# Optimization experiments

Measured on AMD Instinct MI355X. Metric: run time of the kernel, lower is better.

The kernel has to match this reference:

```python
import jax, jax.numpy as jnp
import numpy as np

B, S, H, R, DEPTH = 64, 32, 1024, 256, 9  # batch, seq, hidden, GRU hidden (h//reduction), tree depth


def _gru(x, h, W_ih, W_hh, b_ih, b_hh):
    # PyTorch nn.GRUCell math
    gi = x @ W_ih.T + b_ih
    gh = h @ W_hh.T + b_hh
    i_r, i_z, i_n = jnp.split(gi, 3, axis=-1)
    h_r, h_z, h_n = jnp.split(gh, 3, axis=-1)
    r = jax.nn.sigmoid(i_r + h_r)
    z = jax.nn.sigmoid(i_z + h_z)
    n = jnp.tanh(i_n + r * h_n)
    return (1.0 - z) * n + z * h


def _forward(x, W_hidden, b_hidden, W_hb, b_hb, W_branch, b_branch, W_ih, W_hh, b_ih, b_hh, tree_depth):
    selu = jax.nn.selu
    # root: discretize(selu(hidden(selu(x)))).mean over sequence; discretize=identity (discretize kw None)
    xc = selu(selu(x) @ W_hidden.T + b_hidden).mean(axis=1)[:, None, :]  # [B,1,H]
    hc = jnp.zeros((x.shape[0], 1, W_hh.shape[1]), x.dtype)              # [B,1,R]
    depth = jnp.zeros((x.shape[0], 1, 1), x.dtype)
    for _ in range(tree_depth):  # level-synchronous expansion of the recursive generate()
        hc = _gru(xc, hc, W_ih, W_hh, b_ih, b_hh)
        xh = jnp.concatenate([xc, hc], axis=-1)                          # [B,N,H+R]
        hb = jax.nn.sigmoid(xh @ W_hb.T + b_hb)                          # [B,N,1]
        depth = depth + hb
        lr = selu(xh @ W_branch.T + b_branch)                            # [B,N,2H]
        l, r = jnp.split(lr, 2, axis=-1)
        l = xc - selu(l @ W_hidden.T + b_hidden)                          # residual left child
        r = xc - selu(r @ W_hidden.T + b_hidden)                          # residual right child
        Bn, N, Hd = xc.shape
        xc = jnp.stack([l, r], axis=2).reshape(Bn, 2 * N, Hd)
        hc = jnp.repeat(hc, 2, axis=1)
        depth = jnp.repeat(depth, 2, axis=1)
    # leaf nodes: final controller step; terminal = x (no V head), depth += has_branches
    hc = _gru(xc, hc, W_ih, W_hh, b_ih, b_hh)
    hb = jax.nn.sigmoid(jnp.concatenate([xc, hc], axis=-1) @ W_hb.T + b_hb)
    depth = depth + hb
    return jnp.concatenate([xc, depth], axis=-1)  # [B, 2**D, H+1]: leaf terminals + leaf depths


def setup_inputs() -> dict:
    key = jax.random.key(0)
    ks = jax.random.split(key, 6)
    def w(k, o, i):
        return (jax.random.normal(k, (o, i), jnp.float32) / np.sqrt(i)).astype(jnp.float32)
    return {
        'x': jax.random.normal(ks[0], (B, S, H), jnp.float32),
        'W_hidden': w(ks[1], H, H), 'b_hidden': jnp.zeros((H,), jnp.float32),
        'W_hb': w(ks[2], 1, H + R), 'b_hb': jnp.zeros((1,), jnp.float32),
        'W_branch': w(ks[3], 2 * H, H + R), 'b_branch': jnp.zeros((2 * H,), jnp.float32),
        'W_ih': w(ks[4], 3 * R, H), 'W_hh': w(ks[5], 3 * R, R),
        'b_ih': jnp.zeros((3 * R,), jnp.float32), 'b_hh': jnp.zeros((3 * R,), jnp.float32),
        'tree_depth': DEPTH,
    }


def reference(x, W_hidden, b_hidden, W_hb, b_hb, W_branch, b_branch, W_ih, W_hh, b_ih, b_hh, tree_depth):
    return _forward(x, W_hidden, b_hidden, W_hb, b_hb, W_branch, b_branch, W_ih, W_hh, b_ih, b_hh, tree_depth)
```

## Files before the change

### kernel.cpp

```cpp
#include <hip/hip_runtime.h>
#include <hip/hip_bf16.h>
#include <cstdint>
#include <cstddef>


#define SELU_L 1.0507009873554805f
#define SELU_A 1.6732632423543772f

__device__ __forceinline__ float selu_f(float x) {
    return x > 0.f ? SELU_L * x : (SELU_L * SELU_A) * (__expf(x) - 1.f);
}
__device__ __forceinline__ float sigmoid_f(float x) {
    return 1.f / (1.f + __expf(-x));
}

typedef __attribute__((ext_vector_type(8))) short s16x8;
typedef __attribute__((ext_vector_type(4))) float f32x4;

__device__ __forceinline__ void gld16(const void* g, void* l) {
    __builtin_amdgcn_global_load_lds(
        (const __attribute__((address_space(1))) uint32_t*)g,
        (__attribute__((address_space(3))) uint32_t*)l, 16, 0, 0);
}

enum { AM_PLAIN = 0, AM_CONCAT = 2 };
enum { EP_NONE = 0, EP_SELU32 = 1, EP_BRANCH = 2, EP_RESID = 3 };

template <int AMODE, int EPI>
__device__ __forceinline__ void gemm_body(
    int bm, int bn, int M, int K,
    const __hip_bfloat16* __restrict__ A, int lda,
    const __hip_bfloat16* __restrict__ A2,
    const __hip_bfloat16* __restrict__ W,
    const float* __restrict__ bias,
    void* __restrict__ Cv, int ldc,
    const __hip_bfloat16* __restrict__ P,
    float* __restrict__ C32, int ldc32,
    short* As, short* Bs)
{
    const int tid  = threadIdx.x;
    const int wave = tid >> 6;
    const int lane = tid & 63;

    const short* gA[4]; const short* gA2p[4]; const short* gB[4];
    short* dA[4]; short* dB[4];
#pragma unroll
    for (int r = 0; r < 4; ++r) {
        const int s   = r * 256 + wave * 64 + lane;
        const int row = s >> 3;
        const int pc  = s & 7;
        const int j   = (pc - (row >> 1)) & 7;
        const int ga  = min(bm + row, M - 1);
        if (AMODE == AM_CONCAT) {
            gA[r]   = (const short*)A  + (size_t)ga * 1024 + j * 8;
            gA2p[r] = (const short*)A2 + (size_t)ga * 256  + j * 8;
        } else {
            gA[r]   = (const short*)A + (size_t)ga * lda + j * 8;
            gA2p[r] = nullptr;
        }
        gB[r] = (const short*)W + (size_t)(bn + row) * K + j * 8;
        dA[r] = &As[(size_t)(r * 256 + wave * 64) * 8];
        dB[r] = &Bs[(size_t)(r * 256 + wave * 64) * 8];
    }

    const int wm = (wave >> 1) * 64, wn = (wave & 1) * 64;
    const int l16 = lane & 15, q4 = lane >> 4;
    int aoff[4], boff[4];
#pragma unroll
    for (int i = 0; i < 4; ++i) {
        int ra = wm + i * 16 + l16;
        aoff[i] = ra * 64 + (((q4 + (ra >> 1)) & 7) << 3);
        int rb = wn + i * 16 + l16;
        boff[i] = rb * 64 + (((q4 + (rb >> 1)) & 7) << 3);
    }

    f32x4 acc[4][4] = {};

    for (int k0 = 0; k0 < K; k0 += 64) {
#pragma unroll
        for (int r = 0; r < 4; ++r) {
            const short* ap;
            if (AMODE == AM_CONCAT)
                ap = (k0 < 1024) ? gA[r] + k0 : gA2p[r] + (k0 - 1024);
            else
                ap = gA[r] + k0;
            gld16(ap, dA[r]);
            gld16(gB[r] + k0, dB[r]);
        }
        __syncthreads();

#pragma unroll
        for (int h = 0; h < 2; ++h) {
            const int hx = h << 5;
            s16x8 af[4], bf[4];
#pragma unroll
            for (int i = 0; i < 4; ++i) af[i] = *(const s16x8*)&As[aoff[i] ^ hx];
#pragma unroll
            for (int i = 0; i < 4; ++i) bf[i] = *(const s16x8*)&Bs[boff[i] ^ hx];
#pragma unroll
            for (int mi = 0; mi < 4; ++mi)
#pragma unroll
                for (int ni = 0; ni < 4; ++ni)
                    acc[mi][ni] = __builtin_amdgcn_mfma_f32_16x16x32_bf16(
                        af[mi], bf[ni], acc[mi][ni], 0, 0, 0);
        }
        __syncthreads();
    }

    const int crow0 = bm + wm + q4 * 4;
    const int ccol0 = bn + wn + l16;
#pragma unroll
    for (int mi = 0; mi < 4; ++mi) {
#pragma unroll
        for (int r = 0; r < 4; ++r) {
            const int row = crow0 + mi * 16 + r;
            if (row >= M) continue;
#pragma unroll
            for (int ni = 0; ni < 4; ++ni) {
                const int col = ccol0 + ni * 16;
                float v = acc[mi][ni][r] + bias[col];
                if (EPI == EP_NONE) {
                    ((float*)Cv)[(size_t)row * ldc + col] = v;
                } else if (EPI == EP_SELU32) {
                    ((float*)Cv)[(size_t)row * ldc + col] = selu_f(v);
                } else if (EPI == EP_BRANCH) {
                    const int c = col >> 10, jj = col & 1023;
                    ((__hip_bfloat16*)Cv)[(size_t)(2 * row + c) * 1024 + jj] =
                        __float2bfloat16(selu_f(v));
                } else {
                    const float pv = __bfloat162float(P[(size_t)(row >> 1) * 1024 + col]);
                    const float o = pv - selu_f(v);
                    ((__hip_bfloat16*)Cv)[(size_t)row * 1024 + col] = __float2bfloat16(o);
                    if (C32) C32[(size_t)row * ldc32 + col] = o;
                }
            }
        }
    }
}

template <int AMODE, int EPI>
__global__ __launch_bounds__(256) void mgemm(
    int M, int N, int K,
    const __hip_bfloat16* __restrict__ A, int lda,
    const __hip_bfloat16* __restrict__ A2,
    const __hip_bfloat16* __restrict__ W,
    const float* __restrict__ bias,
    void* __restrict__ Cv, int ldc,
    const __hip_bfloat16* __restrict__ P,
    float* __restrict__ C32, int ldc32)
{
    __shared__ short As[8192];
    __shared__ short Bs[8192];
    int bxi = blockIdx.x, byi = blockIdx.y;
    {
        const int ncol = gridDim.x, nrow = gridDim.y;
        if ((nrow & 7) == 0) {
            const int lin = byi * ncol + bxi;
            const int xcd = lin & 7;
            const int t = lin >> 3;
            const int rows_per = nrow >> 3;
            bxi = t % ncol;
            byi = xcd * rows_per + t / ncol;
        }
    }
    gemm_body<AMODE, EPI>(byi * 128, bxi * 128, M, K, A, lda, A2, W, bias,
                          Cv, ldc, P, C32, ldc32, As, Bs);
}

struct GPair {
    int M0, K0; const __hip_bfloat16* A0; int lda0;
    const __hip_bfloat16* W0; const float* b0; float* C0; int ldc0;
    int M1, K1; const __hip_bfloat16* A1; int lda1;
    const __hip_bfloat16* W1; const float* b1; float* C1; int ldc1;
};
__global__ __launch_bounds__(256) void mgemm_pair(GPair g)
{
    __shared__ short As[8192];
    __shared__ short Bs[8192];
    int bxi = blockIdx.x, byi = blockIdx.y;
    if (blockIdx.z == 0) {
        const int ncol = gridDim.x, nrow = gridDim.y;
        if ((nrow & 7) == 0) {
            const int lin = byi * ncol + bxi;
            const int xcd = lin & 7;
            const int t = lin >> 3;
            const int rows_per = nrow >> 3;
            bxi = t % ncol;
            byi = xcd * rows_per + t / ncol;
        }
        gemm_body<AM_PLAIN, EP_NONE>(byi * 128, bxi * 128, g.M0, g.K0,
                                     g.A0, g.lda0, nullptr, g.W0, g.b0,
                                     g.C0, g.ldc0, nullptr, nullptr, 0, As, Bs);
    } else {
        if (byi * 128 >= g.M1) return;
        gemm_body<AM_PLAIN, EP_NONE>(byi * 128, bxi * 128, g.M1, g.K1,
                                     g.A1, g.lda1, nullptr, g.W1, g.b1,
                                     g.C1, g.ldc1, nullptr, nullptr, 0, As, Bs);
    }
}

template <int AMODE, int EPI>
__device__ __forceinline__ void gemm256_body(
    int bm, int bn, int M, int K,
    const __hip_bfloat16* __restrict__ A, int lda,
    const __hip_bfloat16* __restrict__ A2,
    const __hip_bfloat16* __restrict__ W,
    const float* __restrict__ bias,
    void* __restrict__ Cv, int ldc,
    const __hip_bfloat16* __restrict__ P,
    float* __restrict__ C32, int ldc32,
    short* As, short* Bs)
{
    const int tid  = threadIdx.x;
    const int wave = tid >> 6;
    const int lane = tid & 63;
    const int wm = (wave >> 2) * 128;
    const int wn = (wave & 3) * 64;
    const int l16 = lane & 15, q4 = lane >> 4;

    const short* gA[2]; const short* gA2p[2]; const short* gB[2];
    int dOf[2];
#pragma unroll
    for (int r = 0; r < 2; ++r) {
        const int s   = r * 512 + tid;
        const int row = s >> 2;
        const int pc  = s & 3;
        const int j   = (pc - (row >> 1)) & 3;
        const int ga  = min(bm + row, M - 1);
        if (AMODE == AM_CONCAT) {
            gA[r]   = (const short*)A  + (size_t)ga * 1024 + j * 8;
            gA2p[r] = (const short*)A2 + (size_t)ga * 256  + j * 8;
        } else {
            gA[r]   = (const short*)A + (size_t)ga * lda + j * 8;
            gA2p[r] = nullptr;
        }
        gB[r]  = (const short*)W + (size_t)(bn + row) * K + j * 8;
        dOf[r] = (r * 512 + wave * 64) * 8;
    }

    int aof[8], bof[4];
#pragma unroll
    for (int m = 0; m < 8; ++m) {
        const int ra = wm + m * 16 + l16;
        aof[m] = ra * 32 + (((q4 + (ra >> 1)) & 3) << 3);
    }
#pragma unroll
    for (int n = 0; n < 4; ++n) {
        const int rb = wn + n * 16 + l16;
        bof[n] = rb * 32 + (((q4 + (rb >> 1)) & 3) << 3);
    }

    f32x4 acc[8][4] = {};
    const int NT = K >> 5;

    auto stage = [&](int t) {
        const int k0 = t << 5;
        const int sb = (t & 3) << 13;
#pragma unroll
        for (int r = 0; r < 2; ++r) {
            const short* ap;
            if (AMODE == AM_CONCAT)
                ap = (k0 < 1024) ? gA[r] + k0 : gA2p[r] + (k0 - 1024);
            else
                ap = gA[r] + k0;
            gld16(ap, &As[sb + dOf[r]]);
        }
#pragma unroll
        for (int r = 0; r < 2; ++r) gld16(gB[r] + k0, &Bs[sb + dOf[r]]);
    };

    stage(0); stage(1); stage(2);

#define STEP256(t_, DOISS_, VMS_) do {                                        \
        asm volatile("s_waitcnt vmcnt(" VMS_ ")" ::: "memory");               \
        __builtin_amdgcn_s_barrier();                                         \
        asm volatile("" ::: "memory");      \
        const int cur_ = ((t_) & 3) << 13;                                    \
        s16x8 af_[8], bf_[4];                                                 \
        _Pragma("unroll")                                                     \
        for (int m = 0; m < 8; ++m) af_[m] = *(const s16x8*)&As[cur_ + aof[m]]; \
        _Pragma("unroll")                                                     \
        for (int n = 0; n < 4; ++n) bf_[n] = *(const s16x8*)&Bs[cur_ + bof[n]]; \
        if (DOISS_) stage((t_) + 3);                                          \
        __builtin_amdgcn_s_setprio(1);                                        \
        _Pragma("unroll")                                                     \
        for (int m = 0; m < 8; ++m)                                           \
            _Pragma("unroll")                                                 \
            for (int n = 0; n < 4; ++n)                                       \
                acc[m][n] = __builtin_amdgcn_mfma_f32_16x16x32_bf16(          \
                    af_[m], bf_[n], acc[m][n], 0, 0, 0);                      \
        __builtin_amdgcn_s_setprio(0);                                        \
    } while (0)

    for (int t = 0; t < NT - 3; ++t) STEP256(t, 1, "8");
    STEP256(NT - 3, 0, "8");
    STEP256(NT - 2, 0, "4");
    STEP256(NT - 1, 0, "0");
#undef STEP256

    const int crow0 = bm + wm + q4 * 4;
    const int ccol0 = bn + wn + l16;
#pragma unroll
    for (int m8 = 0; m8 < 8; ++m8) {
#pragma unroll
        for (int r = 0; r < 4; ++r) {
            const int row = crow0 + m8 * 16 + r;
            if (row >= M) continue;
#pragma unroll
            for (int n4 = 0; n4 < 4; ++n4) {
                const int col = ccol0 + n4 * 16;
                float v = acc[m8][n4][r] + bias[col];
                if (EPI == EP_NONE) {
                    ((float*)Cv)[(size_t)row * ldc + col] = v;
                } else if (EPI == EP_SELU32) {
                    ((float*)Cv)[(size_t)row * ldc + col] = selu_f(v);
                } else if (EPI == EP_BRANCH) {
                    const int c = col >> 10, jj = col & 1023;
                    ((__hip_bfloat16*)Cv)[(size_t)(2 * row + c) * 1024 + jj] =
                        __float2bfloat16(selu_f(v));
                } else {
                    const float pv = __bfloat162float(P[(size_t)(row >> 1) * 1024 + col]);
                    const float o = pv - selu_f(v);
                    ((__hip_bfloat16*)Cv)[(size_t)row * 1024 + col] = __float2bfloat16(o);
                    if (C32) C32[(size_t)row * ldc32 + col] = o;
                }
            }
        }
    }
}

template <int AMODE, int EPI>
__global__ __launch_bounds__(512) void mgemm256(
    int M, int N, int K,
    const __hip_bfloat16* __restrict__ A, int lda,
    const __hip_bfloat16* __restrict__ A2,
    const __hip_bfloat16* __restrict__ W,
    const float* __restrict__ bias,
    void* __restrict__ Cv, int ldc,
    const __hip_bfloat16* __restrict__ P,
    float* __restrict__ C32, int ldc32)
{
    __shared__ short As[32768];
    __shared__ short Bs[32768];
    int bxi = blockIdx.x, byi = blockIdx.y;
    {
        const int ncol = gridDim.x, nrow = gridDim.y;
        if ((nrow & 7) == 0) {
            const int lin = byi * ncol + bxi;
            const int xcd = lin & 7;
            const int t = lin >> 3;
            const int rows_per = nrow >> 3;
            bxi = t % ncol;
            byi = xcd * rows_per + t / ncol;
        }
    }
    gemm256_body<AMODE, EPI>(byi * 256, bxi * 256, M, K, A, lda, A2, W, bias,
                             Cv, ldc, P, C32, ldc32, As, Bs);
}

__global__ void cvt4_k(const float* __restrict__ s0, __hip_bfloat16* __restrict__ d0, int n0,
                       const float* __restrict__ s1, __hip_bfloat16* __restrict__ d1, int n1,
                       const float* __restrict__ s2, __hip_bfloat16* __restrict__ d2, int n2,
                       const float* __restrict__ s3, __hip_bfloat16* __restrict__ d3, int n3)
{
    int i = blockIdx.x * 256 + threadIdx.x;
    if (i < n0) { d0[i] = __float2bfloat16(s0[i]); return; }
    i -= n0;
    if (i < n1) { d1[i] = __float2bfloat16(s1[i]); return; }
    i -= n1;
    if (i < n2) { d2[i] = __float2bfloat16(s2[i]); return; }
    i -= n2;
    if (i < n3) { d3[i] = __float2bfloat16(s3[i]); }
}

__global__ void selu_cvt_k(const float* __restrict__ in, __hip_bfloat16* __restrict__ out, int n)
{
    int i = blockIdx.x * 256 + threadIdx.x;
    if (i < n) out[i] = __float2bfloat16(selu_f(in[i]));
}

__global__ void mean_kernel(const float* __restrict__ T, __hip_bfloat16* __restrict__ xc)
{
    const int idx = blockIdx.x * 256 + threadIdx.x;
    const int b = idx >> 10, h = idx & 1023;
    const float* p = T + (size_t)b * 32 * 1024 + h;
    float s = 0.f;
#pragma unroll
    for (int si = 0; si < 32; ++si) s += p[si * 1024];
    xc[idx] = __float2bfloat16(s * (1.f / 32.f));
}

__global__ __launch_bounds__(256) void gateshb_kernel(
    const float* __restrict__ gi,
    const float* __restrict__ gh,
    const float* __restrict__ b_hh,
    const __hip_bfloat16* __restrict__ hold,
    __hip_bfloat16* __restrict__ hnew,
    const __hip_bfloat16* __restrict__ xc,
    const float* __restrict__ W_hb,
    const float* __restrict__ b_hb,
    const float* __restrict__ depth_old,
    float* __restrict__ depth_out, int dstride,
    int first)
{
    const int m = blockIdx.x;
    const int j = threadIdx.x;
    __shared__ float red[4];

    const float* gim = gi + (size_t)m * 768;
    const float ir = gim[j], iz = gim[256 + j], in_ = gim[512 + j];
    float hr, hz, hn, h0;
    if (first) {
        hr = b_hh[j]; hz = b_hh[256 + j]; hn = b_hh[512 + j]; h0 = 0.f;
    } else {
        const float* ghm = gh + (size_t)(m >> 1) * 768;
        hr = ghm[j]; hz = ghm[256 + j]; hn = ghm[512 + j];
        h0 = __bfloat162float(hold[(size_t)(m >> 1) * 256 + j]);
    }
    const float r = sigmoid_f(ir + hr);
    const float z = sigmoid_f(iz + hz);
    const float n = tanhf(in_ + r * hn);
    const float hv = (1.f - z) * n + z * h0;
    hnew[(size_t)m * 256 + j] = __float2bfloat16(hv);

    const __hip_bfloat16* xr = xc + (size_t)m * 1024;
    float s = hv * W_hb[1024 + j];
#pragma unroll
    for (int kk = 0; kk < 4; ++kk) {
        const int k = j + kk * 256;
        s += __bfloat162float(xr[k]) * W_hb[k];
    }
#pragma unroll
    for (int off = 32; off; off >>= 1) s += __shfl_down(s, off);
    if ((j & 63) == 0) red[j >> 6] = s;
    __syncthreads();
    if (j == 0) {
        const float tot = red[0] + red[1] + red[2] + red[3];
        const float hb = sigmoid_f(tot + b_hb[0]);
        const float d0 = first ? 0.f : depth_old[m >> 1];
        depth_out[(size_t)m * dstride] = d0 + hb;
    }
}

extern "C" void kernel_launch(void* const* d_in, const int* in_sizes, int n_in,
                              void* d_out, int out_size, void* d_ws, size_t ws_size,
                              hipStream_t stream)
{
    const float* x        = (const float*)d_in[0];
    const float* W_hidden = (const float*)d_in[1];
    const float* b_hidden = (const float*)d_in[2];
    const float* W_hb     = (const float*)d_in[3];
    const float* b_hb     = (const float*)d_in[4];
    const float* W_branch = (const float*)d_in[5];
    const float* b_branch = (const float*)d_in[6];
    const float* W_ih     = (const float*)d_in[7];
    const float* W_hh     = (const float*)d_in[8];
    const float* b_ih     = (const float*)d_in[9];
    const float* b_hh     = (const float*)d_in[10];

    char* ws = (char*)d_ws;
    size_t off = 0;
    auto alloc = [&](size_t bytes) {
        void* p = ws + off;
        off += (bytes + 255) & ~(size_t)255;
        return p;
    };
    __hip_bfloat16* Whb  = (__hip_bfloat16*)alloc(1024 * 1024 * 2);
    __hip_bfloat16* Wbb  = (__hip_bfloat16*)alloc(2048 * 1280 * 2);
    __hip_bfloat16* Wib  = (__hip_bfloat16*)alloc(768 * 1024 * 2);
    __hip_bfloat16* Whh  = (__hip_bfloat16*)alloc(768 * 256 * 2);
    __hip_bfloat16* Xs   = (__hip_bfloat16*)alloc((size_t)2048 * 1024 * 2);
    float*          GI   = (float*)alloc((size_t)32768 * 768 * 4);
    __hip_bfloat16* U    = (__hip_bfloat16*)alloc((size_t)32768 * 1024 * 2);
    __hip_bfloat16* XC0  = (__hip_bfloat16*)alloc((size_t)32768 * 1024 * 2);
    __hip_bfloat16* XC1  = (__hip_bfloat16*)alloc((size_t)32768 * 1024 * 2);
    __hip_bfloat16* HC0  = (__hip_bfloat16*)alloc((size_t)32768 * 256 * 2);
    __hip_bfloat16* HC1  = (__hip_bfloat16*)alloc((size_t)32768 * 256 * 2);
    float*          D0   = (float*)alloc(32768 * 4);
    float*          D1   = (float*)alloc(32768 * 4);
    float*          GH   = (float*)U;

    float* out = (float*)d_out;

    {
        const int n0 = 1024 * 1024, n1 = 2048 * 1280, n2 = 768 * 1024, n3 = 768 * 256;
        cvt4_k<<<(n0 + n1 + n2 + n3 + 255) / 256, 256, 0, stream>>>(
            W_hidden, Whb, n0, W_branch, Wbb, n1, W_ih, Wib, n2, W_hh, Whh, n3);
    }
    selu_cvt_k<<<(2048 * 1024 + 255) / 256, 256, 0, stream>>>(x, Xs, 2048 * 1024);

    mgemm<AM_PLAIN, EP_SELU32><<<dim3(1024 / 128, 2048 / 128), 256, 0, stream>>>(
        2048, 1024, 1024, Xs, 1024, nullptr, Whb, b_hidden, GI, 1024, nullptr, nullptr, 0);
    mean_kernel<<<(64 * 1024) / 256, 256, 0, stream>>>(GI, XC0);

    __hip_bfloat16* xc_cur = XC0; __hip_bfloat16* xc_next = XC1;
    __hip_bfloat16* hc_prev = nullptr; __hip_bfloat16* hc_new = HC0;
    float* d_prev = nullptr; float* d_next = D0;

    for (int d = 0; d < 9; ++d) {
        const int M = 64 << d;
        GPair g;
        g.M0 = M;     g.K0 = 1024; g.A0 = xc_cur;  g.lda0 = 1024;
        g.W0 = Wib;   g.b0 = b_ih; g.C0 = GI;      g.ldc0 = 768;
        g.M1 = M / 2; g.K1 = 256;  g.A1 = hc_prev; g.lda1 = 256;
        g.W1 = Whh;   g.b1 = b_hh; g.C1 = GH;      g.ldc1 = 768;
        mgemm_pair<<<dim3(768 / 128, (M + 127) / 128, d > 0 ? 2 : 1), 256, 0, stream>>>(g);

        gateshb_kernel<<<M, 256, 0, stream>>>(
            GI, (const float*)GH, b_hh, hc_prev, hc_new,
            xc_cur, W_hb, b_hb, d_prev, d_next, 1, d == 0 ? 1 : 0);

        if (d >= 7) {
            mgemm256<AM_CONCAT, EP_BRANCH><<<dim3(2048 / 256, M / 256), 512, 0, stream>>>(
                M, 2048, 1280, xc_cur, 1024, hc_new, Wbb, b_branch, U, 1024,
                nullptr, nullptr, 0);
            mgemm256<AM_PLAIN, EP_RESID><<<dim3(1024 / 256, (2 * M) / 256), 512, 0, stream>>>(
                2 * M, 1024, 1024, U, 1024, nullptr, Whb, b_hidden, xc_next, 1024,
                xc_cur, d == 8 ? out : nullptr, 1025);
        } else {
            mgemm<AM_CONCAT, EP_BRANCH><<<dim3(2048 / 128, (M + 127) / 128), 256, 0, stream>>>(
                M, 2048, 1280, xc_cur, 1024, hc_new, Wbb, b_branch, U, 1024,
                nullptr, nullptr, 0);
            mgemm<AM_PLAIN, EP_RESID><<<dim3(1024 / 128, (2 * M) / 128), 256, 0, stream>>>(
                2 * M, 1024, 1024, U, 1024, nullptr, Whb, b_hidden, xc_next, 1024,
                xc_cur, d == 8 ? out : nullptr, 1025);
        }

        __hip_bfloat16* t = xc_cur; xc_cur = xc_next; xc_next = t;
        hc_prev = hc_new; hc_new = (hc_new == HC0) ? HC1 : HC0;
        d_prev = d_next;  d_next = (d_next == D0) ? D1 : D0;
    }

    {
        const int M = 32768;
        mgemm256<AM_PLAIN, EP_NONE><<<dim3(768 / 256, M / 256), 512, 0, stream>>>(
            M, 768, 1024, xc_cur, 1024, nullptr, Wib, b_ih, GI, 768,
            nullptr, nullptr, 0);
        mgemm<AM_PLAIN, EP_NONE><<<dim3(768 / 128, (M / 2) / 128), 256, 0, stream>>>(
            M / 2, 768, 256, hc_prev, 256, nullptr, Whh, b_hh, (void*)GH, 768,
            nullptr, nullptr, 0);
        gateshb_kernel<<<M, 256, 0, stream>>>(
            GI, (const float*)GH, b_hh, hc_prev, hc_new,
            xc_cur, W_hb, b_hb, d_prev, out + 1024, 1025, 0);
    }
}
```

Baseline: 1.469 ms.

## Fuse tree levels 0-4 into one persistent kernel with grid barriers

```diff
diff --git a/kernel.cpp b/kernel.cpp
--- a/kernel.cpp
+++ b/kernel.cpp
@@ -274,7 +274,7 @@
 #define STEP256(t_, DOISS_, VMS_) do {                                        \
         asm volatile("s_waitcnt vmcnt(" VMS_ ")" ::: "memory");               \
         __builtin_amdgcn_s_barrier();                                         \
-        asm volatile("" ::: "memory");      \
+        asm volatile("" ::: "memory");                                        \
         const int cur_ = ((t_) & 3) << 13;                                    \
         s16x8 af_[8], bf_[4];                                                 \
         _Pragma("unroll")                                                     \
@@ -358,55 +358,17 @@
                              Cv, ldc, P, C32, ldc32, As, Bs);
 }
 
-__global__ void cvt4_k(const float* __restrict__ s0, __hip_bfloat16* __restrict__ d0, int n0,
-                       const float* __restrict__ s1, __hip_bfloat16* __restrict__ d1, int n1,
-                       const float* __restrict__ s2, __hip_bfloat16* __restrict__ d2, int n2,
-                       const float* __restrict__ s3, __hip_bfloat16* __restrict__ d3, int n3)
-{
-    int i = blockIdx.x * 256 + threadIdx.x;
-    if (i < n0) { d0[i] = __float2bfloat16(s0[i]); return; }
-    i -= n0;
-    if (i < n1) { d1[i] = __float2bfloat16(s1[i]); return; }
-    i -= n1;
-    if (i < n2) { d2[i] = __float2bfloat16(s2[i]); return; }
-    i -= n2;
-    if (i < n3) { d3[i] = __float2bfloat16(s3[i]); }
-}
-
-__global__ void selu_cvt_k(const float* __restrict__ in, __hip_bfloat16* __restrict__ out, int n)
-{
-    int i = blockIdx.x * 256 + threadIdx.x;
-    if (i < n) out[i] = __float2bfloat16(selu_f(in[i]));
-}
-
-__global__ void mean_kernel(const float* __restrict__ T, __hip_bfloat16* __restrict__ xc)
-{
-    const int idx = blockIdx.x * 256 + threadIdx.x;
-    const int b = idx >> 10, h = idx & 1023;
-    const float* p = T + (size_t)b * 32 * 1024 + h;
-    float s = 0.f;
-#pragma unroll
-    for (int si = 0; si < 32; ++si) s += p[si * 1024];
-    xc[idx] = __float2bfloat16(s * (1.f / 32.f));
-}
-
-__global__ __launch_bounds__(256) void gateshb_kernel(
-    const float* __restrict__ gi,
-    const float* __restrict__ gh,
+__device__ __forceinline__ void gates_row(
+    int m, int first,
+    const float* __restrict__ gi, const float* __restrict__ gh,
     const float* __restrict__ b_hh,
-    const __hip_bfloat16* __restrict__ hold,
-    __hip_bfloat16* __restrict__ hnew,
+    const __hip_bfloat16* __restrict__ hold, __hip_bfloat16* __restrict__ hnew,
     const __hip_bfloat16* __restrict__ xc,
-    const float* __restrict__ W_hb,
-    const float* __restrict__ b_hb,
-    const float* __restrict__ depth_old,
-    float* __restrict__ depth_out, int dstride,
-    int first)
-{
-    const int m = blockIdx.x;
+    const float* __restrict__ W_hb, const float* __restrict__ b_hb,
+    const float* __restrict__ depth_old, float* __restrict__ depth_out,
+    int dstride, float* red)
+{
     const int j = threadIdx.x;
-    __shared__ float red[4];
-
     const float* gim = gi + (size_t)m * 768;
     const float ir = gim[j], iz = gim[256 + j], in_ = gim[512 + j];
     float hr, hz, hn, h0;
@@ -440,6 +402,153 @@
         const float d0 = first ? 0.f : depth_old[m >> 1];
         depth_out[(size_t)m * dstride] = d0 + hb;
     }
+    __syncthreads();
+}
+
+__global__ __launch_bounds__(256) void gateshb_kernel(
+    const float* __restrict__ gi, const float* __restrict__ gh,
+    const float* __restrict__ b_hh,
+    const __hip_bfloat16* __restrict__ hold, __hip_bfloat16* __restrict__ hnew,
+    const __hip_bfloat16* __restrict__ xc,
+    const float* __restrict__ W_hb, const float* __restrict__ b_hb,
+    const float* __restrict__ depth_old, float* __restrict__ depth_out,
+    int dstride, int first)
+{
+    __shared__ float red[4];
+    gates_row(blockIdx.x, first, gi, gh, b_hh, hold, hnew, xc, W_hb, b_hb,
+              depth_old, depth_out, dstride, red);
+}
+
+__device__ __forceinline__ void grid_barrier(unsigned* bar)
+{
+    __syncthreads();
+    if (threadIdx.x == 0) {
+        __threadfence();
+        const unsigned gen = __hip_atomic_load(&bar[1], __ATOMIC_RELAXED,
+                                               __HIP_MEMORY_SCOPE_AGENT);
+        const unsigned n = __hip_atomic_fetch_add(&bar[0], 1u, __ATOMIC_ACQ_REL,
+                                                  __HIP_MEMORY_SCOPE_AGENT);
+        if (n + 1u == gridDim.x) {
+            __hip_atomic_store(&bar[0], 0u, __ATOMIC_RELAXED,
+                               __HIP_MEMORY_SCOPE_AGENT);
+            __hip_atomic_fetch_add(&bar[1], 1u, __ATOMIC_RELEASE,
+                                   __HIP_MEMORY_SCOPE_AGENT);
+        } else {
+            while (__hip_atomic_load(&bar[1], __ATOMIC_ACQUIRE,
+                                     __HIP_MEMORY_SCOPE_AGENT) == gen)
+                __builtin_amdgcn_s_sleep(8);
+        }
+        __threadfence();
+    }
+    __syncthreads();
+}
+
+struct L04Args {
+    const __hip_bfloat16 *Wib, *Whh, *Wbb, *Whb;
+    const float *b_ih, *b_hh, *b_branch, *b_hidden, *W_hb, *b_hb;
+    __hip_bfloat16 *XC0, *XC1, *HC0, *HC1, *U;
+    float *D0, *D1, *GI, *GH;
+    unsigned *bar;
+};
+
+__global__ __launch_bounds__(256) void levels04_kernel(L04Args a)
+{
+    __shared__ short As[8192];
+    __shared__ short Bs[8192];
+    __shared__ float red[4];
+
+    __hip_bfloat16* xc_cur = a.XC0; __hip_bfloat16* xc_next = a.XC1;
+    __hip_bfloat16* hc_prev = nullptr; __hip_bfloat16* hc_new = a.HC0;
+    float* d_prev = nullptr; float* d_next = a.D0;
+
+    for (int d = 0; d < 5; ++d) {
+        const int M  = 64 << d;
+        const int gy = (M + 127) >> 7;
+
+        {
+            const int t1  = gy * 6;
+            const int gy2 = ((M >> 1) + 127) >> 7;
+            const int tot = t1 + (d > 0 ? gy2 * 6 : 0);
+            for (int t = blockIdx.x; t < tot; t += gridDim.x) {
+                if (t < t1)
+                    gemm_body<AM_PLAIN, EP_NONE>((t / 6) * 128, (t % 6) * 128,
+                        M, 1024, xc_cur, 1024, nullptr, a.Wib, a.b_ih,
+                        a.GI, 768, nullptr, nullptr, 0, As, Bs);
+                else {
+                    const int u = t - t1;
+                    gemm_body<AM_PLAIN, EP_NONE>((u / 6) * 128, (u % 6) * 128,
+                        M >> 1, 256, hc_prev, 256, nullptr, a.Whh, a.b_hh,
+                        a.GH, 768, nullptr, nullptr, 0, As, Bs);
+                }
+                __syncthreads();
+            }
+            grid_barrier(a.bar);
+        }
+
+        for (int m = blockIdx.x; m < M; m += gridDim.x)
+            gates_row(m, d == 0 ? 1 : 0, a.GI, a.GH, a.b_hh, hc_prev, hc_new,
+                      xc_cur, a.W_hb, a.b_hb, d_prev, d_next, 1, red);
+        grid_barrier(a.bar);
+
+        {
+            const int tot = 16 * gy;
+            for (int t = blockIdx.x; t < tot; t += gridDim.x) {
+                gemm_body<AM_CONCAT, EP_BRANCH>((t / 16) * 128, (t % 16) * 128,
+                    M, 1280, xc_cur, 1024, hc_new, a.Wbb, a.b_branch,
+                    a.U, 1024, nullptr, nullptr, 0, As, Bs);
+                __syncthreads();
+            }
+            grid_barrier(a.bar);
+        }
+
+        {
+            const int gy4 = ((2 * M) + 127) >> 7;
+            const int tot = 8 * gy4;
+            for (int t = blockIdx.x; t < tot; t += gridDim.x) {
+                gemm_body<AM_PLAIN, EP_RESID>((t / 8) * 128, (t % 8) * 128,
+                    2 * M, 1024, a.U, 1024, nullptr, a.Whb, a.b_hidden,
+                    xc_next, 1024, xc_cur, nullptr, 0, As, Bs);
+                __syncthreads();
+            }
+            grid_barrier(a.bar);
+        }
+
+        __hip_bfloat16* tx = xc_cur; xc_cur = xc_next; xc_next = tx;
+        hc_prev = hc_new; hc_new = (hc_new == a.HC0) ? a.HC1 : a.HC0;
+        d_prev = d_next;  d_next = (d_next == a.D0) ? a.D1 : a.D0;
+    }
+}
+
+__global__ void cvt4_k(const float* __restrict__ s0, __hip_bfloat16* __restrict__ d0, int n0,
+                       const float* __restrict__ s1, __hip_bfloat16* __restrict__ d1, int n1,
+                       const float* __restrict__ s2, __hip_bfloat16* __restrict__ d2, int n2,
+                       const float* __restrict__ s3, __hip_bfloat16* __restrict__ d3, int n3)
+{
+    int i = blockIdx.x * 256 + threadIdx.x;
+    if (i < n0) { d0[i] = __float2bfloat16(s0[i]); return; }
+    i -= n0;
+    if (i < n1) { d1[i] = __float2bfloat16(s1[i]); return; }
+    i -= n1;
+    if (i < n2) { d2[i] = __float2bfloat16(s2[i]); return; }
+    i -= n2;
+    if (i < n3) { d3[i] = __float2bfloat16(s3[i]); }
+}
+
+__global__ void selu_cvt_k(const float* __restrict__ in, __hip_bfloat16* __restrict__ out, int n)
+{
+    int i = blockIdx.x * 256 + threadIdx.x;
+    if (i < n) out[i] = __float2bfloat16(selu_f(in[i]));
+}
+
+__global__ void mean_kernel(const float* __restrict__ T, __hip_bfloat16* __restrict__ xc)
+{
+    const int idx = blockIdx.x * 256 + threadIdx.x;
+    const int b = idx >> 10, h = idx & 1023;
+    const float* p = T + (size_t)b * 32 * 1024 + h;
+    float s = 0.f;
+#pragma unroll
+    for (int si = 0; si < 32; ++si) s += p[si * 1024];
+    xc[idx] = __float2bfloat16(s * (1.f / 32.f));
 }
 
 extern "C" void kernel_launch(void* const* d_in, const int* in_sizes, int n_in,
@@ -478,9 +587,12 @@
     __hip_bfloat16* HC1  = (__hip_bfloat16*)alloc((size_t)32768 * 256 * 2);
     float*          D0   = (float*)alloc(32768 * 4);
     float*          D1   = (float*)alloc(32768 * 4);
+    unsigned*       BAR  = (unsigned*)alloc(256);
     float*          GH   = (float*)U;
 
     float* out = (float*)d_out;
+
+    hipMemsetAsync(BAR, 0, 8, stream);
 
     {
         const int n0 = 1024 * 1024, n1 = 2048 * 1280, n2 = 768 * 1024, n3 = 768 * 256;
@@ -493,22 +605,32 @@
         2048, 1024, 1024, Xs, 1024, nullptr, Whb, b_hidden, GI, 1024, nullptr, nullptr, 0);
     mean_kernel<<<(64 * 1024) / 256, 256, 0, stream>>>(GI, XC0);
 
-    __hip_bfloat16* xc_cur = XC0; __hip_bfloat16* xc_next = XC1;
-    __hip_bfloat16* hc_prev = nullptr; __hip_bfloat16* hc_new = HC0;
-    float* d_prev = nullptr; float* d_next = D0;
-
-    for (int d = 0; d < 9; ++d) {
+    {
+        L04Args la;
+        la.Wib = Wib; la.Whh = Whh; la.Wbb = Wbb; la.Whb = Whb;
+        la.b_ih = b_ih; la.b_hh = b_hh; la.b_branch = b_branch;
+        la.b_hidden = b_hidden; la.W_hb = W_hb; la.b_hb = b_hb;
+        la.XC0 = XC0; la.XC1 = XC1; la.HC0 = HC0; la.HC1 = HC1; la.U = U;
+        la.D0 = D0; la.D1 = D1; la.GI = GI; la.GH = GH; la.bar = BAR;
+        levels04_kernel<<<128, 256, 0, stream>>>(la);
+    }
+
+    __hip_bfloat16* xc_cur = XC1; __hip_bfloat16* xc_next = XC0;
+    __hip_bfloat16* hc_prev = HC0; __hip_bfloat16* hc_new = HC1;
+    float* d_prev = D0; float* d_next = D1;
+
+    for (int d = 5; d < 9; ++d) {
         const int M = 64 << d;
         GPair g;
         g.M0 = M;     g.K0 = 1024; g.A0 = xc_cur;  g.lda0 = 1024;
         g.W0 = Wib;   g.b0 = b_ih; g.C0 = GI;      g.ldc0 = 768;
         g.M1 = M / 2; g.K1 = 256;  g.A1 = hc_prev; g.lda1 = 256;
         g.W1 = Whh;   g.b1 = b_hh; g.C1 = GH;      g.ldc1 = 768;
-        mgemm_pair<<<dim3(768 / 128, (M + 127) / 128, d > 0 ? 2 : 1), 256, 0, stream>>>(g);
+        mgemm_pair<<<dim3(768 / 128, (M + 127) / 128, 2), 256, 0, stream>>>(g);
 
         gateshb_kernel<<<M, 256, 0, stream>>>(
             GI, (const float*)GH, b_hh, hc_prev, hc_new,
-            xc_cur, W_hb, b_hb, d_prev, d_next, 1, d == 0 ? 1 : 0);
+            xc_cur, W_hb, b_hb, d_prev, d_next, 1, 0);
 
         if (d >= 7) {
             mgemm256<AM_CONCAT, EP_BRANCH><<<dim3(2048 / 256, M / 256), 512, 0, stream>>>(
```

After: 2.035 ms. 38.6% more time.
